# Kernel optimization log

Hardware: AMD Instinct MI355X
Metric: run time of the kernel (lower is better)

Reference implementation:

```python
import jax, jax.numpy as jnp
import numpy as np

N_GRAPHS = 500
NODES_PER_GRAPH = 200
EDGES_PER_GRAPH = 6400
N = N_GRAPHS * NODES_PER_GRAPH          # 100000 nodes
E = N_GRAPHS * EDGES_PER_GRAPH          # 3200000 edges
D = 256                                  # dim_hidden
RATIO = 0.8
EPS = 1e-12


def setup_inputs() -> dict:
    key = jax.random.key(0)
    k1, k2 = jax.random.split(key, 2)
    x = jax.random.normal(k1, (N, D), dtype=jnp.float32)
    # edges consistent with batch: both endpoints inside the same graph
    rng = np.random.default_rng(0)
    g = np.repeat(np.arange(N_GRAPHS, dtype=np.int32), EDGES_PER_GRAPH)
    row = g * NODES_PER_GRAPH + rng.integers(0, NODES_PER_GRAPH, E).astype(np.int32)
    col = g * NODES_PER_GRAPH + rng.integers(0, NODES_PER_GRAPH, E).astype(np.int32)
    edge_index = jnp.asarray(np.stack([row, col]), dtype=jnp.int32)
    batch = jnp.asarray(np.repeat(np.arange(N_GRAPHS, dtype=np.int32), NODES_PER_GRAPH))
    W = jax.random.normal(k2, (2 * D, 1), dtype=jnp.float32) * (1.0 / np.sqrt(2 * D))
    b = jnp.zeros((1,), dtype=jnp.float32)
    return {"x": x, "edge_index": edge_index, "batch": batch, "W": W, "b": b}


def _edge_scores(x, W, b, edge_index):
    # concat(x[row], x[col]) @ W == (x @ W_row)[row] + (x @ W_col)[col]
    # -> avoids materializing the [E, 2D] edge_rep tensor.
    row, col = edge_index[0], edge_index[1]
    s_row = x @ W[:D, 0]   # [N]
    s_col = x @ W[D:, 0]   # [N]
    return s_row[row] + s_col[col] + b[0]  # [E]


def _topk_edge_mask(edge_score, edge_graph):
    # sparse_sort (descending=True): norm = minmax(score) - graph_id; argsort desc.
    f_min, f_max = edge_score.min(), edge_score.max()
    norm = (edge_score - f_min) / (f_max - f_min + EPS) - edge_graph.astype(edge_score.dtype)
    perm = jnp.argsort(-norm)  # graphs ascending, score descending within graph
    deg = jax.ops.segment_sum(jnp.ones_like(edge_graph), edge_graph, num_segments=N_GRAPHS)
    k = jnp.ceil(RATIO * deg.astype(jnp.float32)).astype(deg.dtype)
    start = jnp.concatenate([jnp.zeros((1,), deg.dtype), jnp.cumsum(deg)[:-1]])
    sg = edge_graph[perm]                        # graph id in sorted order
    pos = jnp.arange(E, dtype=deg.dtype) - start[sg]  # rank within segment
    keep_sorted = pos < k[sg]
    # scatter keep flags back to original edge order
    return jnp.zeros((E,), dtype=bool).at[perm].set(keep_sorted)


def _relabel(x, batch, edge_index, emask):
    # padded equivalent of torch.unique + scatter relabel:
    # selected nodes are compacted to the front of x/batch; dropped slots -> -1.
    row, col = edge_index[0], edge_index[1]
    m = emask.astype(jnp.int32)
    sel = (jnp.zeros((N,), jnp.int32).at[row].max(m).at[col].max(m)).astype(bool)
    new_id = jnp.where(sel, jnp.cumsum(sel) - 1, -1)           # [N]
    new_ei = jnp.where(emask[None, :], new_id[edge_index], -1)  # [2, E], -1 = padding
    order = jnp.argsort(~sel)                                   # stable: selected first
    x_out = x[order]                                            # [N, D], selected at front
    batch_out = jnp.where(sel[order], batch[order], -1)
    return x_out, new_ei, batch_out, sel.sum()


def reference(x, edge_index, batch, W, b):
    edge_score = _edge_scores(x, W, b, edge_index)
    edge_graph = batch[edge_index[0]]
    mask = _topk_edge_mask(edge_score, edge_graph)   # True = causal edge
    causal_w = jnp.where(mask, edge_score, 0.0)
    conf_w = jnp.where(mask, 0.0, -edge_score)
    causal_x, causal_ei, causal_batch, n_causal = _relabel(x, batch, edge_index, mask)
    conf_x, conf_ei, conf_batch, n_conf = _relabel(x, batch, edge_index, ~mask)
    return (causal_x, causal_ei, causal_w, causal_batch, n_causal,
            conf_x, conf_ei, conf_w, conf_batch, n_conf,
            edge_score, mask)
```

## Files before the change

### kernel.cpp

```cpp
#include <hip/hip_runtime.h>
#include <cmath>

typedef unsigned long long u64;
typedef unsigned int u32;
typedef unsigned char u8;

#define DHID 256
#define NMAX 100000
#define EMAX 3200000
#define EPGMAX 6400
#define NBLKMAX 128
#define TOPK_T 512

__device__ float g_srow[NMAX];
__device__ float g_scol[NMAX];
__device__ float g_escore[EMAX];
__device__ int   g_destC[NMAX];
__device__ int   g_destF[NMAX];
__device__ u8    g_selC[NMAX];
__device__ u8    g_selF[NMAX];
__device__ u8    g_mask[EMAX];
__device__ float g_pmin[1024];
__device__ float g_pmax[1024];
__device__ int   g_blkC[NBLKMAX];
__device__ int   g_blkF[NBLKMAX];
__device__ int   g_tot[2];

__global__ void k_node_scores(const float* __restrict__ x, const float* __restrict__ W, int N){
  int t = blockIdx.x*256 + threadIdx.x;
  if (t < N){ g_selC[t] = 0; g_selF[t] = 0; }
  int lane = threadIdx.x & 63, wave = threadIdx.x >> 6;
  int n = blockIdx.x*4 + wave;
  if (n >= N) return;
  float4 xv = ((const float4*)(x + (size_t)n*DHID))[lane];
  float4 wr = ((const float4*)W)[lane];
  float4 wc = ((const float4*)W)[64 + lane];
  double dr = (double)xv.x*wr.x + (double)xv.y*wr.y + (double)xv.z*wr.z + (double)xv.w*wr.w;
  double dc = (double)xv.x*wc.x + (double)xv.y*wc.y + (double)xv.z*wc.z + (double)xv.w*wc.w;
  #pragma unroll
  for (int off = 32; off; off >>= 1){
    dr += __shfl_xor(dr, off);
    dc += __shfl_xor(dc, off);
  }
  if (lane == 0){ g_srow[n] = (float)dr; g_scol[n] = (float)dc; }
}

__global__ void k_minmax_part(const int* __restrict__ ei, const float* __restrict__ b, int E){
  float b0 = b[0];
  float lmin = INFINITY, lmax = -INFINITY;
  for (int e = blockIdx.x*256 + threadIdx.x; e < E; e += gridDim.x*256){
    int r = ei[e], c = ei[E + e];
    float s = (g_srow[r] + g_scol[c]) + b0;
    g_escore[e] = s;
    lmin = fminf(lmin, s); lmax = fmaxf(lmax, s);
  }
  __shared__ float smin[256], smax[256];
  smin[threadIdx.x] = lmin; smax[threadIdx.x] = lmax;
  __syncthreads();
  for (int st = 128; st; st >>= 1){
    if (threadIdx.x < st){
      smin[threadIdx.x] = fminf(smin[threadIdx.x], smin[threadIdx.x+st]);
      smax[threadIdx.x] = fmaxf(smax[threadIdx.x], smax[threadIdx.x+st]);
    }
    __syncthreads();
  }
  if (threadIdx.x == 0){ g_pmin[blockIdx.x] = smin[0]; g_pmax[blockIdx.x] = smax[0]; }
}

__global__ __launch_bounds__(TOPK_T) void k_topk(const int* __restrict__ ei,
    float* __restrict__ out, long long oCW, long long oFW, long long oS, long long oM,
    int E, int EPG, int k){
  __shared__ u32 keys[EPGMAX];
  __shared__ u8  keep[EPGMAX];
  __shared__ int hist[256];
  __shared__ int scan[256];
  __shared__ int tscan[TOPK_T];
  __shared__ float redA[TOPK_T];
  __shared__ u32 sh_prefix;
  __shared__ int sh_rem, sh_rem_next, sh_digit;
  int g = blockIdx.x, tid = threadIdx.x;
  long long base = (long long)g * EPG;

  float lmin = fminf(g_pmin[tid], g_pmin[tid + 512]);
  float lmax = fmaxf(g_pmax[tid], g_pmax[tid + 512]);
  redA[tid] = lmin;
  __syncthreads();
  for (int st = 256; st; st >>= 1){
    if (tid < st) redA[tid] = fminf(redA[tid], redA[tid+st]);
    __syncthreads();
  }
  float fmin = redA[0];
  __syncthreads();
  redA[tid] = lmax;
  __syncthreads();
  for (int st = 256; st; st >>= 1){
    if (tid < st) redA[tid] = fmaxf(redA[tid], redA[tid+st]);
    __syncthreads();
  }
  float fmax = redA[0];
  __syncthreads();

  float denom = (fmax - fmin) + 1e-12f;
  float gf = (float)g;

  for (int i = tid; i < EPG; i += TOPK_T){
    float s = g_escore[base + i];
    float frac = (s - fmin) / denom;
    float nk = frac - gf;
    u32 u = __float_as_uint(nk);
    u = (u & 0x80000000u) ? ~u : (u | 0x80000000u);
    keys[i] = ~u;
  }
  if (tid == 0){ sh_prefix = 0; sh_rem = k; }
  __syncthreads();

  for (int shift = 24; shift >= 0; shift -= 8){
    if (tid < 256) hist[tid] = 0;
    __syncthreads();
    u32 pref = sh_prefix;
    int lane = tid & 63;
    for (int i = tid; i < EPG; i += TOPK_T){
      u32 kk = keys[i];
      bool cand = (shift == 24) || ((kk >> (shift + 8)) == pref);
      if (cand){
        u32 digit = (kk >> shift) & 0xFF;
        u32 d0 = __builtin_amdgcn_readfirstlane(digit);
        if (__all(digit == d0)){
          u64 m = __ballot(1);
          if (lane == __builtin_ctzll(m)) atomicAdd(&hist[d0], (int)__popcll(m));
        } else {
          atomicAdd(&hist[digit], 1);
        }
      }
    }
    __syncthreads();
    if (tid < 256) scan[tid] = hist[tid];
    __syncthreads();
    for (int st = 1; st < 256; st <<= 1){
      int t2 = (tid < 256 && tid >= st) ? scan[tid - st] : 0;
      __syncthreads();
      if (tid < 256) scan[tid] += t2;
      __syncthreads();
    }
    if (tid < 256){
      int rem = sh_rem;
      int cumprev = tid ? scan[tid - 1] : 0;
      if (cumprev < rem && rem <= scan[tid]){
        sh_digit = tid;
        sh_rem_next = rem - cumprev;
      }
    }
    __syncthreads();
    if (tid == 0){
      sh_prefix = (sh_prefix << 8) | (u32)sh_digit;
      sh_rem = sh_rem_next;
    }
    __syncthreads();
  }
  u32 T = sh_prefix;
  int r_budget = sh_rem;

  int CH = (EPG + TOPK_T - 1) / TOPK_T;
  int c0 = tid * CH;
  int cnt = 0;
  for (int j = 0; j < CH; j++){
    int i = c0 + j;
    if (i < EPG && keys[i] == T) cnt++;
  }
  tscan[tid] = cnt;
  __syncthreads();
  for (int st = 1; st < TOPK_T; st <<= 1){
    int t2 = (tid >= st) ? tscan[tid - st] : 0;
    __syncthreads();
    tscan[tid] += t2;
    __syncthreads();
  }
  int rank = tid ? tscan[tid - 1] : 0;

  for (int j = 0; j < CH; j++){
    int i = c0 + j;
    if (i >= EPG) break;
    u32 kk = keys[i];
    int kept;
    if (kk < T) kept = 1;
    else if (kk == T){ kept = (rank < r_budget); rank++; }
    else kept = 0;
    keep[i] = (u8)kept;
  }
  __syncthreads();

  for (int i = tid; i < EPG; i += TOPK_T){
    long long e = base + i;
    int kept = keep[i];
    float s = g_escore[e];
    int rr = ei[e], cc = ei[E + e];
    g_mask[e] = (u8)kept;
    out[oS + e]  = s;
    out[oM + e]  = kept ? 1.0f : 0.0f;
    out[oCW + e] = kept ? s : 0.0f;
    out[oFW + e] = kept ? 0.0f : -s;
    if (kept){ g_selC[rr] = 1; g_selC[cc] = 1; }
    else     { g_selF[rr] = 1; g_selF[cc] = 1; }
  }
}

__global__ void k_blocksum(int N){
  int bb = blockIdx.x, tid = threadIdx.x;
  int start = bb*1024;
  int c = 0, f = 0;
  #pragma unroll
  for (int q = 0; q < 4; q++){
    int n = start + tid*4 + q;
    if (n < N){ c += g_selC[n]; f += g_selF[n]; }
  }
  __shared__ int sc[256], sf[256];
  sc[tid] = c; sf[tid] = f;
  __syncthreads();
  for (int st = 128; st; st >>= 1){
    if (tid < st){ sc[tid] += sc[tid+st]; sf[tid] += sf[tid+st]; }
    __syncthreads();
  }
  if (tid == 0){ g_blkC[bb] = sc[0]; g_blkF[bb] = sf[0]; }
}

__global__ void k_scanblk(int nb, float* __restrict__ out, long long oNC, long long oNF){
  __shared__ int sC[NBLKMAX], sF[NBLKMAX];
  int tid = threadIdx.x;
  int c = (tid < nb) ? g_blkC[tid] : 0;
  int f = (tid < nb) ? g_blkF[tid] : 0;
  sC[tid] = c; sF[tid] = f;
  __syncthreads();
  for (int st = 1; st < NBLKMAX; st <<= 1){
    int a  = (tid >= st) ? sC[tid - st] : 0;
    int b2 = (tid >= st) ? sF[tid - st] : 0;
    __syncthreads();
    sC[tid] += a; sF[tid] += b2;
    __syncthreads();
  }
  if (tid < nb){ g_blkC[tid] = sC[tid] - c; g_blkF[tid] = sF[tid] - f; }
  if (tid == NBLKMAX - 1){
    g_tot[0] = sC[NBLKMAX-1]; g_tot[1] = sF[NBLKMAX-1];
    out[oNC] = (float)sC[NBLKMAX-1];
    out[oNF] = (float)sF[NBLKMAX-1];
  }
}

__global__ void k_dest(const int* __restrict__ batch,
    float* __restrict__ out, long long oCB, long long oFB, int N){
  int bb = blockIdx.x, tid = threadIdx.x;
  int start = bb*1024;
  int idx0 = start + tid*4;
  int c[4], f[4]; int sc = 0, sf = 0;
  #pragma unroll
  for (int q = 0; q < 4; q++){
    int n = idx0 + q;
    int vc = (n < N) ? (int)g_selC[n] : 0;
    int vf = (n < N) ? (int)g_selF[n] : 0;
    c[q] = vc; f[q] = vf; sc += vc; sf += vf;
  }
  __shared__ int xc[256], xf[256];
  xc[tid] = sc; xf[tid] = sf;
  __syncthreads();
  for (int st = 1; st < 256; st <<= 1){
    int ac = (tid >= st) ? xc[tid-st] : 0;
    int af = (tid >= st) ? xf[tid-st] : 0;
    __syncthreads();
    xc[tid] += ac; xf[tid] += af;
    __syncthreads();
  }
  int excC = ((tid ? xc[tid-1] : 0)) + g_blkC[bb];
  int excF = ((tid ? xf[tid-1] : 0)) + g_blkF[bb];
  int nC = g_tot[0], nF = g_tot[1];
  int runC = 0, runF = 0;
  #pragma unroll
  for (int q = 0; q < 4; q++){
    int n = idx0 + q;
    if (n >= N) break;
    runC += c[q]; runF += f[q];
    int cumC = excC + runC;
    int cumF = excF + runF;
    int dC = c[q] ? (cumC - 1) : (nC + (n - cumC));
    int dF = f[q] ? (cumF - 1) : (nF + (n - cumF));
    dC = min(max(dC, 0), N-1);
    dF = min(max(dF, 0), N-1);
    g_destC[n] = dC; g_destF[n] = dF;
    float bt = (float)batch[n];
    out[oCB + dC] = c[q] ? bt : -1.0f;
    out[oFB + dF] = f[q] ? bt : -1.0f;
  }
}

__global__ void k_ei_out(const int* __restrict__ ei,
    float* __restrict__ out, long long oCE, long long oFE, int E){
  int e = blockIdx.x*256 + threadIdx.x;
  if (e >= E) return;
  int r = ei[e], c = ei[E + e];
  int m = g_mask[e];
  out[oCE + e]     = m ? (float)g_destC[r] : -1.0f;
  out[oCE + E + e] = m ? (float)g_destC[c] : -1.0f;
  out[oFE + e]     = m ? -1.0f : (float)g_destF[r];
  out[oFE + E + e] = m ? -1.0f : (float)g_destF[c];
}

__global__ void k_x_out(const float* __restrict__ x, float* __restrict__ out,
    long long oCX, long long oFX, int N){
  long long t = (long long)blockIdx.x*256 + threadIdx.x;
  if (t >= (long long)N*64) return;
  int n = (int)(t >> 6), cq = (int)(t & 63);
  float4 v = ((const float4*)x)[(long long)n*64 + cq];
  int dC = g_destC[n], dF = g_destF[n];
  long long iC = oCX + (long long)dC*DHID + cq*4;
  *reinterpret_cast<float4*>(out + iC) = v;
  long long iF = oFX + (long long)dF*DHID + cq*4;
  out[iF] = v.x;
  float2 mid; mid.x = v.y; mid.y = v.z;
  *reinterpret_cast<float2*>(out + iF + 1) = mid;
  out[iF + 3] = v.w;
}

extern "C" void kernel_launch(void* const* d_in, const int* in_sizes, int n_in,
                              void* d_out, int out_size, void* d_ws, size_t ws_size,
                              hipStream_t stream) {
  const float* x   = (const float*)d_in[0];
  const int* ei    = (const int*)d_in[1];
  const int* batch = (const int*)d_in[2];
  const float* W   = (const float*)d_in[3];
  const float* b   = (const float*)d_in[4];
  float* out = (float*)d_out;

  int N   = in_sizes[0] / DHID;
  int E   = in_sizes[1] / 2;
  if (N > NMAX) N = NMAX;
  if (E > EMAX) E = EMAX;
  const int G   = N / 200;
  int EPG = (G > 0) ? E / G : 0;
  if (EPG > EPGMAX) EPG = EPGMAX;
  const int k   = (int)ceilf(0.8f * (float)EPG);

  long long oCX = 0;
  long long oCE = oCX + (long long)N*DHID;
  long long oCW = oCE + 2LL*E;
  long long oCB = oCW + E;
  long long oNC = oCB + N;
  long long oFX = oNC + 1;
  long long oFE = oFX + (long long)N*DHID;
  long long oFW = oFE + 2LL*E;
  long long oFB = oFW + E;
  long long oNF = oFB + N;
  long long oS  = oNF + 1;
  long long oM  = oS + E;

  k_node_scores<<<(N + 3)/4, 256, 0, stream>>>(x, W, N);
  k_minmax_part<<<1024, 256, 0, stream>>>(ei, b, E);
  k_topk<<<G, TOPK_T, 0, stream>>>(ei, out, oCW, oFW, oS, oM, E, EPG, k);
  int nblk = (N + 1023)/1024;
  k_blocksum<<<nblk, 256, 0, stream>>>(N);
  k_scanblk<<<1, NBLKMAX, 0, stream>>>(nblk, out, oNC, oNF);
  k_dest<<<nblk, 256, 0, stream>>>(batch, out, oCB, oFB, N);
  k_ei_out<<<(E + 255)/256, 256, 0, stream>>>(ei, out, oCE, oFE, E);
  k_x_out<<<(int)(((long long)N*64 + 255)/256), 256, 0, stream>>>(x, out, oCX, oFX, N);
}
```

Baseline: 171.3 us.

## Use wave-shuffle reductions/scans and fuse edge and row-gather output kernels

Replaces the shared-memory tree reductions and Hillis-Steele scans in the minmax, topk, blocksum, scanblk and dest kernels with wave-level shuffle reductions and scans plus a small cross-wave combine. This cuts the number of barriers and LDS traffic. The edge-index output kernel and the x-permutation kernel are merged into one launch. The x copy is inverted into a gather: an inverse destination map is written, so each output row reads its source row. This makes the output writes contiguous, at the cost of scattered reads and an extra inverse-index array.

```diff
diff --git a/kernel.cpp b/kernel.cpp
--- a/kernel.cpp
+++ b/kernel.cpp
@@ -17,6 +17,8 @@
 __device__ float g_escore[EMAX];
 __device__ int   g_destC[NMAX];
 __device__ int   g_destF[NMAX];
+__device__ int   g_invC[NMAX];
+__device__ int   g_invF[NMAX];
 __device__ u8    g_selC[NMAX];
 __device__ u8    g_selF[NMAX];
 __device__ u8    g_mask[EMAX];
@@ -54,17 +56,20 @@
     g_escore[e] = s;
     lmin = fminf(lmin, s); lmax = fmaxf(lmax, s);
   }
-  __shared__ float smin[256], smax[256];
-  smin[threadIdx.x] = lmin; smax[threadIdx.x] = lmax;
-  __syncthreads();
-  for (int st = 128; st; st >>= 1){
-    if (threadIdx.x < st){
-      smin[threadIdx.x] = fminf(smin[threadIdx.x], smin[threadIdx.x+st]);
-      smax[threadIdx.x] = fmaxf(smax[threadIdx.x], smax[threadIdx.x+st]);
-    }
-    __syncthreads();
-  }
-  if (threadIdx.x == 0){ g_pmin[blockIdx.x] = smin[0]; g_pmax[blockIdx.x] = smax[0]; }
+  #pragma unroll
+  for (int off = 32; off; off >>= 1){
+    lmin = fminf(lmin, __shfl_xor(lmin, off));
+    lmax = fmaxf(lmax, __shfl_xor(lmax, off));
+  }
+  __shared__ float smin[4], smax[4];
+  int lane = threadIdx.x & 63, wid = threadIdx.x >> 6;
+  if (lane == 0){ smin[wid] = lmin; smax[wid] = lmax; }
+  __syncthreads();
+  if (threadIdx.x == 0){
+    float m0 = fminf(fminf(smin[0], smin[1]), fminf(smin[2], smin[3]));
+    float m1 = fmaxf(fmaxf(smax[0], smax[1]), fmaxf(smax[2], smax[3]));
+    g_pmin[blockIdx.x] = m0; g_pmax[blockIdx.x] = m1;
+  }
 }
 
 __global__ __launch_bounds__(TOPK_T) void k_topk(const int* __restrict__ ei,
@@ -73,32 +78,29 @@
   __shared__ u32 keys[EPGMAX];
   __shared__ u8  keep[EPGMAX];
   __shared__ int hist[256];
-  __shared__ int scan[256];
-  __shared__ int tscan[TOPK_T];
-  __shared__ float redA[TOPK_T];
+  __shared__ float wred[8], wred2[8];
+  __shared__ int wsum[8];
   __shared__ u32 sh_prefix;
   __shared__ int sh_rem, sh_rem_next, sh_digit;
   int g = blockIdx.x, tid = threadIdx.x;
+  int lane = tid & 63, wid = tid >> 6;
   long long base = (long long)g * EPG;
 
   float lmin = fminf(g_pmin[tid], g_pmin[tid + 512]);
   float lmax = fmaxf(g_pmax[tid], g_pmax[tid + 512]);
-  redA[tid] = lmin;
-  __syncthreads();
-  for (int st = 256; st; st >>= 1){
-    if (tid < st) redA[tid] = fminf(redA[tid], redA[tid+st]);
-    __syncthreads();
-  }
-  float fmin = redA[0];
-  __syncthreads();
-  redA[tid] = lmax;
-  __syncthreads();
-  for (int st = 256; st; st >>= 1){
-    if (tid < st) redA[tid] = fmaxf(redA[tid], redA[tid+st]);
-    __syncthreads();
-  }
-  float fmax = redA[0];
-  __syncthreads();
+  #pragma unroll
+  for (int off = 32; off; off >>= 1){
+    lmin = fminf(lmin, __shfl_xor(lmin, off));
+    lmax = fmaxf(lmax, __shfl_xor(lmax, off));
+  }
+  if (lane == 0){ wred[wid] = lmin; wred2[wid] = lmax; }
+  if (tid == 0){ sh_prefix = 0; sh_rem = k; }
+  __syncthreads();
+  float fmin = wred[0], fmax = wred2[0];
+  #pragma unroll
+  for (int w = 1; w < 8; w++){
+    fmin = fminf(fmin, wred[w]); fmax = fmaxf(fmax, wred2[w]);
+  }
 
   float denom = (fmax - fmin) + 1e-12f;
   float gf = (float)g;
@@ -111,14 +113,10 @@
     u = (u & 0x80000000u) ? ~u : (u | 0x80000000u);
     keys[i] = ~u;
   }
-  if (tid == 0){ sh_prefix = 0; sh_rem = k; }
-  __syncthreads();
-
   for (int shift = 24; shift >= 0; shift -= 8){
     if (tid < 256) hist[tid] = 0;
     __syncthreads();
     u32 pref = sh_prefix;
-    int lane = tid & 63;
     for (int i = tid; i < EPG; i += TOPK_T){
       u32 kk = keys[i];
       bool cand = (shift == 24) || ((kk >> (shift + 8)) == pref);
@@ -134,18 +132,25 @@
       }
     }
     __syncthreads();
-    if (tid < 256) scan[tid] = hist[tid];
-    __syncthreads();
-    for (int st = 1; st < 256; st <<= 1){
-      int t2 = (tid < 256 && tid >= st) ? scan[tid - st] : 0;
-      __syncthreads();
-      if (tid < 256) scan[tid] += t2;
-      __syncthreads();
+    int v = 0, inc = 0;
+    if (tid < 256){
+      v = hist[tid];
+      inc = v;
+      #pragma unroll
+      for (int off = 1; off < 64; off <<= 1){
+        int t2 = __shfl_up(inc, off);
+        if (lane >= off) inc += t2;
+      }
+      if (lane == 63) wsum[wid] = inc;
     }
+    __syncthreads();
     if (tid < 256){
+      int wpre = 0;
+      for (int w = 0; w < wid; w++) wpre += wsum[w];
+      int incl = inc + wpre;
+      int cumprev = incl - v;
       int rem = sh_rem;
-      int cumprev = tid ? scan[tid - 1] : 0;
-      if (cumprev < rem && rem <= scan[tid]){
+      if (cumprev < rem && rem <= incl){
         sh_digit = tid;
         sh_rem_next = rem - cumprev;
       }
@@ -167,15 +172,17 @@
     int i = c0 + j;
     if (i < EPG && keys[i] == T) cnt++;
   }
-  tscan[tid] = cnt;
-  __syncthreads();
-  for (int st = 1; st < TOPK_T; st <<= 1){
-    int t2 = (tid >= st) ? tscan[tid - st] : 0;
-    __syncthreads();
-    tscan[tid] += t2;
-    __syncthreads();
-  }
-  int rank = tid ? tscan[tid - 1] : 0;
+  int inc2 = cnt;
+  #pragma unroll
+  for (int off = 1; off < 64; off <<= 1){
+    int t2 = __shfl_up(inc2, off);
+    if (lane >= off) inc2 += t2;
+  }
+  if (lane == 63) wsum[wid] = inc2;
+  __syncthreads();
+  int wpre2 = 0;
+  for (int w = 0; w < wid; w++) wpre2 += wsum[w];
+  int rank = inc2 - cnt + wpre2;
 
   for (int j = 0; j < CH; j++){
     int i = c0 + j;
@@ -213,35 +220,41 @@
     int n = start + tid*4 + q;
     if (n < N){ c += g_selC[n]; f += g_selF[n]; }
   }
-  __shared__ int sc[256], sf[256];
-  sc[tid] = c; sf[tid] = f;
-  __syncthreads();
-  for (int st = 128; st; st >>= 1){
-    if (tid < st){ sc[tid] += sc[tid+st]; sf[tid] += sf[tid+st]; }
-    __syncthreads();
-  }
-  if (tid == 0){ g_blkC[bb] = sc[0]; g_blkF[bb] = sf[0]; }
+  #pragma unroll
+  for (int off = 32; off; off >>= 1){
+    c += __shfl_xor(c, off); f += __shfl_xor(f, off);
+  }
+  __shared__ int sc[4], sf[4];
+  int lane = tid & 63, wid = tid >> 6;
+  if (lane == 0){ sc[wid] = c; sf[wid] = f; }
+  __syncthreads();
+  if (tid == 0){
+    g_blkC[bb] = sc[0]+sc[1]+sc[2]+sc[3];
+    g_blkF[bb] = sf[0]+sf[1]+sf[2]+sf[3];
+  }
 }
 
 __global__ void k_scanblk(int nb, float* __restrict__ out, long long oNC, long long oNF){
-  __shared__ int sC[NBLKMAX], sF[NBLKMAX];
+  __shared__ int wsC[2], wsF[2];
   int tid = threadIdx.x;
+  int lane = tid & 63, wid = tid >> 6;
   int c = (tid < nb) ? g_blkC[tid] : 0;
   int f = (tid < nb) ? g_blkF[tid] : 0;
-  sC[tid] = c; sF[tid] = f;
-  __syncthreads();
-  for (int st = 1; st < NBLKMAX; st <<= 1){
-    int a  = (tid >= st) ? sC[tid - st] : 0;
-    int b2 = (tid >= st) ? sF[tid - st] : 0;
-    __syncthreads();
-    sC[tid] += a; sF[tid] += b2;
-    __syncthreads();
-  }
-  if (tid < nb){ g_blkC[tid] = sC[tid] - c; g_blkF[tid] = sF[tid] - f; }
+  int ic = c, iff = f;
+  #pragma unroll
+  for (int off = 1; off < 64; off <<= 1){
+    int a = __shfl_up(ic, off), b2 = __shfl_up(iff, off);
+    if (lane >= off){ ic += a; iff += b2; }
+  }
+  if (lane == 63){ wsC[wid] = ic; wsF[wid] = iff; }
+  __syncthreads();
+  int pc = (wid == 1) ? wsC[0] : 0;
+  int pf = (wid == 1) ? wsF[0] : 0;
+  if (tid < nb){ g_blkC[tid] = ic - c + pc; g_blkF[tid] = iff - f + pf; }
   if (tid == NBLKMAX - 1){
-    g_tot[0] = sC[NBLKMAX-1]; g_tot[1] = sF[NBLKMAX-1];
-    out[oNC] = (float)sC[NBLKMAX-1];
-    out[oNF] = (float)sF[NBLKMAX-1];
+    g_tot[0] = ic + pc; g_tot[1] = iff + pf;
+    out[oNC] = (float)(ic + pc);
+    out[oNF] = (float)(iff + pf);
   }
 }
 
@@ -258,18 +271,20 @@
     int vf = (n < N) ? (int)g_selF[n] : 0;
     c[q] = vc; f[q] = vf; sc += vc; sf += vf;
   }
-  __shared__ int xc[256], xf[256];
-  xc[tid] = sc; xf[tid] = sf;
-  __syncthreads();
-  for (int st = 1; st < 256; st <<= 1){
-    int ac = (tid >= st) ? xc[tid-st] : 0;
-    int af = (tid >= st) ? xf[tid-st] : 0;
-    __syncthreads();
-    xc[tid] += ac; xf[tid] += af;
-    __syncthreads();
-  }
-  int excC = ((tid ? xc[tid-1] : 0)) + g_blkC[bb];
-  int excF = ((tid ? xf[tid-1] : 0)) + g_blkF[bb];
+  int lane = tid & 63, wid = tid >> 6;
+  int ic = sc, iff = sf;
+  #pragma unroll
+  for (int off = 1; off < 64; off <<= 1){
+    int a = __shfl_up(ic, off), b2 = __shfl_up(iff, off);
+    if (lane >= off){ ic += a; iff += b2; }
+  }
+  __shared__ int wsC[4], wsF[4];
+  if (lane == 63){ wsC[wid] = ic; wsF[wid] = iff; }
+  __syncthreads();
+  int wpreC = 0, wpreF = 0;
+  for (int w = 0; w < wid; w++){ wpreC += wsC[w]; wpreF += wsF[w]; }
+  int excC = (ic - sc + wpreC) + g_blkC[bb];
+  int excF = (iff - sf + wpreF) + g_blkF[bb];
   int nC = g_tot[0], nF = g_tot[1];
   int runC = 0, runF = 0;
   #pragma unroll
@@ -284,38 +299,44 @@
     dC = min(max(dC, 0), N-1);
     dF = min(max(dF, 0), N-1);
     g_destC[n] = dC; g_destF[n] = dF;
+    g_invC[dC] = n; g_invF[dF] = n;
     float bt = (float)batch[n];
     out[oCB + dC] = c[q] ? bt : -1.0f;
     out[oFB + dF] = f[q] ? bt : -1.0f;
   }
 }
 
-__global__ void k_ei_out(const int* __restrict__ ei,
-    float* __restrict__ out, long long oCE, long long oFE, int E){
-  int e = blockIdx.x*256 + threadIdx.x;
-  if (e >= E) return;
-  int r = ei[e], c = ei[E + e];
-  int m = g_mask[e];
-  out[oCE + e]     = m ? (float)g_destC[r] : -1.0f;
-  out[oCE + E + e] = m ? (float)g_destC[c] : -1.0f;
-  out[oFE + e]     = m ? -1.0f : (float)g_destF[r];
-  out[oFE + E + e] = m ? -1.0f : (float)g_destF[c];
-}
-
-__global__ void k_x_out(const float* __restrict__ x, float* __restrict__ out,
-    long long oCX, long long oFX, int N){
-  long long t = (long long)blockIdx.x*256 + threadIdx.x;
-  if (t >= (long long)N*64) return;
-  int n = (int)(t >> 6), cq = (int)(t & 63);
-  float4 v = ((const float4*)x)[(long long)n*64 + cq];
-  int dC = g_destC[n], dF = g_destF[n];
-  long long iC = oCX + (long long)dC*DHID + cq*4;
-  *reinterpret_cast<float4*>(out + iC) = v;
-  long long iF = oFX + (long long)dF*DHID + cq*4;
-  out[iF] = v.x;
-  float2 mid; mid.x = v.y; mid.y = v.z;
-  *reinterpret_cast<float2*>(out + iF + 1) = mid;
-  out[iF + 3] = v.w;
+__global__ void k_out(const int* __restrict__ ei, const float* __restrict__ x,
+    float* __restrict__ out, long long oCE, long long oFE,
+    long long oCX, long long oFX, int E, int N, int EB){
+  int bid = blockIdx.x, tid = threadIdx.x;
+  if (bid < EB){
+    int e = bid*256 + tid;
+    if (e >= E) return;
+    int r = ei[e], c = ei[E + e];
+    int m = g_mask[e];
+    out[oCE + e]     = m ? (float)g_destC[r] : -1.0f;
+    out[oCE + E + e] = m ? (float)g_destC[c] : -1.0f;
+    out[oFE + e]     = m ? -1.0f : (float)g_destF[r];
+    out[oFE + E + e] = m ? -1.0f : (float)g_destF[c];
+    return;
+  }
+  int row = (bid - EB)*4 + (tid >> 6);
+  int cq  = tid & 63;
+  if (row < N){
+    int src = g_invC[row];
+    float4 v = ((const float4*)(x + (size_t)src*DHID))[cq];
+    *reinterpret_cast<float4*>(out + oCX + (long long)row*DHID + cq*4) = v;
+  } else if (row < 2*N){
+    int m = row - N;
+    int src = g_invF[m];
+    float4 v = ((const float4*)(x + (size_t)src*DHID))[cq];
+    long long iF = oFX + (long long)m*DHID + cq*4;
+    out[iF] = v.x;
+    float2 mid; mid.x = v.y; mid.y = v.z;
+    *reinterpret_cast<float2*>(out + iF + 1) = mid;
+    out[iF + 3] = v.w;
+  }
 }
 
 extern "C" void kernel_launch(void* const* d_in, const int* in_sizes, int n_in,
@@ -357,6 +378,7 @@
   k_blocksum<<<nblk, 256, 0, stream>>>(N);
   k_scanblk<<<1, NBLKMAX, 0, stream>>>(nblk, out, oNC, oNF);
   k_dest<<<nblk, 256, 0, stream>>>(batch, out, oCB, oFB, N);
-  k_ei_out<<<(E + 255)/256, 256, 0, stream>>>(ei, out, oCE, oFE, E);
-  k_x_out<<<(int)(((long long)N*64 + 255)/256), 256, 0, stream>>>(x, out, oCX, oFX, N);
-}
+  int EB = (E + 255)/256;
+  int XB = (2*N + 3)/4;
+  k_out<<<EB + XB, 256, 0, stream>>>(ei, x, out, oCE, oFE, oCX, oFX, E, N, EB);
+}
```

Result: no change. 173.3 us (+1.1%).
